# Performance work log

Measured on AMD Instinct MI355X. Metric: run time of the kernel, lower is better.

The kernel has to match this reference:

```python
import jax, jax.numpy as jnp
import numpy as np

# TDNN with context [-2, 2], full_context=True -> kernel_width 5.
# The original per-timestep index_select + tiny conv1d loop is, for full context,
# exactly a single VALID 1D convolution over time, followed by ReLU.

B, T, D_IN, D_OUT, KW = 32, 1024, 512, 512, 5


def setup_inputs() -> dict:
    key = jax.random.key(0)
    k1, k2, k3 = jax.random.split(key, 3)
    stdv = 1.0 / np.sqrt(D_IN)
    x = jax.random.normal(k1, (B, T, D_IN), dtype=jnp.float32)
    kernel = jax.random.normal(k2, (D_OUT, D_IN, KW), dtype=jnp.float32) * stdv
    bias = jax.random.normal(k3, (D_OUT,), dtype=jnp.float32) * stdv
    return {"x": x, "kernel": kernel, "bias": bias}


def reference(x, kernel, bias):
    # x: [B, T, D_in] -> [B, D_in, T] to match torch conv1d layout
    xc = jnp.transpose(x, (0, 2, 1))
    # VALID conv over time; kernel layout OIW matches torch (out, in, width)
    out = jax.lax.conv_general_dilated(
        xc, kernel,
        window_strides=(1,),
        padding="VALID",
        dimension_numbers=("NCW", "OIW", "NCW"),
    )  # [B, D_out, T - KW + 1]
    out = out + bias[None, :, None]
    return jax.nn.relu(out)
```

## Files before the change

kernel.cpp:

```cpp
#include <hip/hip_runtime.h>
#include <stdint.h>

#define BATCH 32
#define TLEN  1024
#define DIN   512
#define DOUT  512
#define KW    5
#define TOUT  1020
#define KDIM  (DIN * KW)

#define BM 128
#define BN 128
#define BK 64

typedef __attribute__((ext_vector_type(8))) short bf16x8;
typedef __attribute__((ext_vector_type(4))) float f32x4;

__device__ __forceinline__ uint16_t f2bf(float f) {
    uint32_t u = __float_as_uint(f);
    uint32_t r = u + 0x7FFFu + ((u >> 16) & 1u);
    return (uint16_t)(r >> 16);
}

__global__ void convert_pack(const float4* __restrict__ x, uint4* __restrict__ xb,
                             const float* __restrict__ w, uint16_t* __restrict__ wb) {
    int bid = blockIdx.x;
    if (bid < 8192) {
        int idx = bid * 256 + threadIdx.x;
        float4 a = x[2 * idx];
        float4 b = x[2 * idx + 1];
        uint4 v;
        v.x = (uint32_t)f2bf(a.x) | ((uint32_t)f2bf(a.y) << 16);
        v.y = (uint32_t)f2bf(a.z) | ((uint32_t)f2bf(a.w) << 16);
        v.z = (uint32_t)f2bf(b.x) | ((uint32_t)f2bf(b.y) << 16);
        v.w = (uint32_t)f2bf(b.z) | ((uint32_t)f2bf(b.w) << 16);
        xb[idx] = v;
    } else {
        int idx = (bid - 8192) * 256 + threadIdx.x;
        int o   = idx / KDIM;
        int rem = idx - o * KDIM;
        int k   = rem >> 9;
        int i   = rem & 511;
        wb[idx] = f2bf(w[(o * DIN + i) * KW + k]);
    }
}

__global__ void __launch_bounds__(256, 4)
tdnn_gemm(const uint16_t* __restrict__ xb,
          const uint16_t* __restrict__ wb,
          const float* __restrict__ bias,
          float* __restrict__ out) {
    __shared__ uint16_t As[BM * BK];
    __shared__ uint16_t Bs[BN * BK];

    const int j    = blockIdx.x;
    const int xcd  = j & 7;
    const int nb   = (j >> 3) & 3;
    const int gi   = j >> 5;
    const int g    = gi * 8 + xcd;
    const int b    = g >> 3;
    const int tb   = g & 7;
    const int t0   = tb * BM;
    const int n0   = nb * BN;

    const int tid  = threadIdx.x;
    const int lane = tid & 63;
    const int w    = tid >> 6;
    const int m_wave = (w & 1) * 64;
    const int n_wave = (w >> 1) * 64;

    const uint16_t* xrow = xb + (size_t)b * TLEN * DIN + (size_t)t0 * DIN;
    const uint16_t* wrow = wb + (size_t)n0 * KDIM;

    f32x4 acc[4][4] = {};

    const int ml = lane & 15;
    const int kg = lane >> 4;

    for (int kb = 0; kb < KDIM; kb += BK) {
        #pragma unroll
        for (int i = 0; i < 4; ++i) {
            int c    = w * 256 + i * 64 + lane;
            int row  = c >> 3;
            int slot = c & 7;
            int ccg  = slot ^ (row & 7);
            const uint16_t* gp = xrow + row * DIN + kb + ccg * 8;
            const uint16_t* lp = &As[(w * 256 + i * 64) * 8];
            __builtin_amdgcn_global_load_lds(
                (const __attribute__((address_space(1))) void*)gp,
                (__attribute__((address_space(3))) void*)lp, 16, 0, 0);
        }
        #pragma unroll
        for (int i = 0; i < 4; ++i) {
            int c    = w * 256 + i * 64 + lane;
            int row  = c >> 3;
            int slot = c & 7;
            int ccg  = slot ^ (row & 7);
            const uint16_t* gp = wrow + (size_t)row * KDIM + kb + ccg * 8;
            const uint16_t* lp = &Bs[(w * 256 + i * 64) * 8];
            __builtin_amdgcn_global_load_lds(
                (const __attribute__((address_space(1))) void*)gp,
                (__attribute__((address_space(3))) void*)lp, 16, 0, 0);
        }
        __syncthreads();

        #pragma unroll
        for (int h = 0; h < 2; ++h) {
            const int cc = h * 4 + kg;
            bf16x8 af[4], bfr[4];
            #pragma unroll
            for (int mi = 0; mi < 4; ++mi) {
                int r = m_wave + mi * 16 + ml;
                af[mi] = *(const bf16x8*)&As[r * BK + (cc ^ (r & 7)) * 8];
            }
            #pragma unroll
            for (int ni = 0; ni < 4; ++ni) {
                int r = n_wave + ni * 16 + ml;
                bfr[ni] = *(const bf16x8*)&Bs[r * BK + (cc ^ (r & 7)) * 8];
            }
            #pragma unroll
            for (int mi = 0; mi < 4; ++mi)
                #pragma unroll
                for (int ni = 0; ni < 4; ++ni)
                    acc[mi][ni] = __builtin_amdgcn_mfma_f32_16x16x32_bf16(
                        af[mi], bfr[ni], acc[mi][ni], 0, 0, 0);
        }
        __syncthreads();
    }

    const int rq = (lane >> 4) * 4;
    #pragma unroll
    for (int ni = 0; ni < 4; ++ni) {
        int o = n0 + n_wave + ni * 16 + ml;
        float bv = bias[o];
        float* orow = out + ((size_t)b * DOUT + o) * TOUT;
        #pragma unroll
        for (int mi = 0; mi < 4; ++mi) {
            int tbase = t0 + m_wave + mi * 16 + rq;
            #pragma unroll
            for (int r = 0; r < 4; ++r) {
                int t = tbase + r;
                if (t < TOUT) {
                    float v = acc[mi][ni][r] + bv;
                    orow[t] = v > 0.0f ? v : 0.0f;
                }
            }
        }
    }
}

extern "C" void kernel_launch(void* const* d_in, const int* in_sizes, int n_in,
                              void* d_out, int out_size, void* d_ws, size_t ws_size,
                              hipStream_t stream) {
    const float* x    = (const float*)d_in[0];
    const float* wgt  = (const float*)d_in[1];
    const float* bias = (const float*)d_in[2];
    float* out = (float*)d_out;

    uint16_t* xb = (uint16_t*)d_ws;
    uint16_t* wb = (uint16_t*)((char*)d_ws + (size_t)BATCH * TLEN * DIN * 2);

    convert_pack<<<13312, 256, 0, stream>>>((const float4*)x, (uint4*)xb, wgt, wb);
    tdnn_gemm<<<1024, 256, 0, stream>>>(xb, wb, bias, out);
}
```

Measured before the change: 203.0 us.

## Load GEMM weight fragments directly from global, double BK, coalesce weight packing

```diff
diff --git a/kernel.cpp b/kernel.cpp
--- a/kernel.cpp
+++ b/kernel.cpp
@@ -11,7 +11,7 @@
 
 #define BM 128
 #define BN 128
-#define BK 64
+#define BK 128
 
 typedef __attribute__((ext_vector_type(8))) short bf16x8;
 typedef __attribute__((ext_vector_type(4))) float f32x4;
@@ -24,6 +24,7 @@
 
 __global__ void convert_pack(const float4* __restrict__ x, uint4* __restrict__ xb,
                              const float* __restrict__ w, uint16_t* __restrict__ wb) {
+    __shared__ uint16_t sW[KDIM];
     int bid = blockIdx.x;
     if (bid < 8192) {
         int idx = bid * 256 + threadIdx.x;
@@ -36,12 +37,20 @@
         v.w = (uint32_t)f2bf(b.z) | ((uint32_t)f2bf(b.w) << 16);
         xb[idx] = v;
     } else {
-        int idx = (bid - 8192) * 256 + threadIdx.x;
-        int o   = idx / KDIM;
-        int rem = idx - o * KDIM;
-        int k   = rem >> 9;
-        int i   = rem & 511;
-        wb[idx] = f2bf(w[(o * DIN + i) * KW + k]);
+        int o = bid - 8192;
+        #pragma unroll
+        for (int r = 0; r < 10; ++r) {
+            int idx = r * 256 + threadIdx.x;
+            sW[idx] = f2bf(w[o * KDIM + idx]);
+        }
+        __syncthreads();
+        #pragma unroll
+        for (int r = 0; r < 10; ++r) {
+            int kk = r * 256 + threadIdx.x;
+            int i = kk & 511;
+            int k = kk >> 9;
+            wb[o * KDIM + kk] = sW[i * 5 + k];
+        }
     }
 }
 
@@ -51,7 +60,6 @@
           const float* __restrict__ bias,
           float* __restrict__ out) {
     __shared__ uint16_t As[BM * BK];
-    __shared__ uint16_t Bs[BN * BK];
 
     const int j    = blockIdx.x;
     const int xcd  = j & 7;
@@ -70,34 +78,26 @@
     const int n_wave = (w >> 1) * 64;
 
     const uint16_t* xrow = xb + (size_t)b * TLEN * DIN + (size_t)t0 * DIN;
-    const uint16_t* wrow = wb + (size_t)n0 * KDIM;
-
-    f32x4 acc[4][4] = {};
 
     const int ml = lane & 15;
     const int kg = lane >> 4;
 
+    const uint16_t* bp0 = wb + (size_t)(n0 + n_wave +  0 + ml) * KDIM + kg * 8;
+    const uint16_t* bp1 = wb + (size_t)(n0 + n_wave + 16 + ml) * KDIM + kg * 8;
+    const uint16_t* bp2 = wb + (size_t)(n0 + n_wave + 32 + ml) * KDIM + kg * 8;
+    const uint16_t* bp3 = wb + (size_t)(n0 + n_wave + 48 + ml) * KDIM + kg * 8;
+
+    f32x4 acc[4][4] = {};
+
     for (int kb = 0; kb < KDIM; kb += BK) {
         #pragma unroll
-        for (int i = 0; i < 4; ++i) {
-            int c    = w * 256 + i * 64 + lane;
-            int row  = c >> 3;
-            int slot = c & 7;
-            int ccg  = slot ^ (row & 7);
+        for (int i = 0; i < 8; ++i) {
+            int c    = w * 512 + i * 64 + lane;
+            int row  = c >> 4;
+            int slot = c & 15;
+            int ccg  = slot ^ (row & 15);
             const uint16_t* gp = xrow + row * DIN + kb + ccg * 8;
-            const uint16_t* lp = &As[(w * 256 + i * 64) * 8];
-            __builtin_amdgcn_global_load_lds(
-                (const __attribute__((address_space(1))) void*)gp,
-                (__attribute__((address_space(3))) void*)lp, 16, 0, 0);
-        }
-        #pragma unroll
-        for (int i = 0; i < 4; ++i) {
-            int c    = w * 256 + i * 64 + lane;
-            int row  = c >> 3;
-            int slot = c & 7;
-            int ccg  = slot ^ (row & 7);
-            const uint16_t* gp = wrow + (size_t)row * KDIM + kb + ccg * 8;
-            const uint16_t* lp = &Bs[(w * 256 + i * 64) * 8];
+            const uint16_t* lp = &As[(w * 512 + i * 64) * 8];
             __builtin_amdgcn_global_load_lds(
                 (const __attribute__((address_space(1))) void*)gp,
                 (__attribute__((address_space(3))) void*)lp, 16, 0, 0);
@@ -105,18 +105,18 @@
         __syncthreads();
 
         #pragma unroll
-        for (int h = 0; h < 2; ++h) {
+        for (int h = 0; h < 4; ++h) {
             const int cc = h * 4 + kg;
-            bf16x8 af[4], bfr[4];
+            bf16x8 bfr[4];
+            bfr[0] = *(const bf16x8*)(bp0 + kb + h * 32);
+            bfr[1] = *(const bf16x8*)(bp1 + kb + h * 32);
+            bfr[2] = *(const bf16x8*)(bp2 + kb + h * 32);
+            bfr[3] = *(const bf16x8*)(bp3 + kb + h * 32);
+            bf16x8 af[4];
             #pragma unroll
             for (int mi = 0; mi < 4; ++mi) {
                 int r = m_wave + mi * 16 + ml;
-                af[mi] = *(const bf16x8*)&As[r * BK + (cc ^ (r & 7)) * 8];
-            }
-            #pragma unroll
-            for (int ni = 0; ni < 4; ++ni) {
-                int r = n_wave + ni * 16 + ml;
-                bfr[ni] = *(const bf16x8*)&Bs[r * BK + (cc ^ (r & 7)) * 8];
+                af[mi] = *(const bf16x8*)&As[r * BK + ((cc ^ (r & 15)) * 8)];
             }
             #pragma unroll
             for (int mi = 0; mi < 4; ++mi)
@@ -160,6 +160,6 @@
     uint16_t* xb = (uint16_t*)d_ws;
     uint16_t* wb = (uint16_t*)((char*)d_ws + (size_t)BATCH * TLEN * DIN * 2);
 
-    convert_pack<<<13312, 256, 0, stream>>>((const float4*)x, (uint4*)xb, wgt, wb);
+    convert_pack<<<8704, 256, 0, stream>>>((const float4*)x, (uint4*)xb, wgt, wb);
     tdnn_gemm<<<1024, 256, 0, stream>>>(xb, wb, bias, out);
 }
```

Measured after the change: 349.0 us. +71.9%, slower.
